# Performance work log

Hardware: AMD Instinct MI355X
Metric: run time of the kernel (lower is better)

## Reference

```python
import jax, jax.numpy as jnp
import numpy as np

D_X, D_H, N_I = 1024, 64, 16  # model dim, per-head dim (d_q=d_k=d_v), heads
BSZ, SEQ = 2, 2048


def _linear(x, W, b):
    return x @ W.T + b


def setup_inputs() -> dict:
    key = jax.random.key(0)
    ks = jax.random.split(key, 16)
    s_in = 1.0 / np.sqrt(D_X)
    s_hd = 1.0 / np.sqrt(N_I * D_H)
    return {
        "query": jax.random.normal(ks[0], (BSZ, SEQ, D_X), jnp.float32),
        "key": jax.random.normal(ks[1], (BSZ, SEQ, D_X), jnp.float32),
        "value": jax.random.normal(ks[2], (BSZ, SEQ, D_X), jnp.float32),
        "Wq": jax.random.normal(ks[3], (N_I * D_H, D_X), jnp.float32) * s_in,
        "bq": jnp.zeros((N_I * D_H,), jnp.float32),
        "Wk": jax.random.normal(ks[4], (N_I * D_H, D_X), jnp.float32) * s_in,
        "bk": jnp.zeros((N_I * D_H,), jnp.float32),
        "Wv": jax.random.normal(ks[5], (N_I * D_H, D_X), jnp.float32) * s_in,
        "bv": jnp.zeros((N_I * D_H,), jnp.float32),
        "Wxv": jax.random.normal(ks[6], (N_I * D_H, D_X), jnp.float32) * s_in,
        "bxv": jnp.zeros((N_I * D_H,), jnp.float32),
        "Wxo": jax.random.normal(ks[7], (D_X, N_I * D_H), jnp.float32) * s_hd,
        "bxo": jnp.zeros((D_X,), jnp.float32),
        "Wmo": jax.random.normal(ks[8], (D_X, N_I * D_H), jnp.float32) * s_hd,
        "bmo": jnp.zeros((D_X,), jnp.float32),
    }


def reference(query, key, value, Wq, bq, Wk, bk, Wv, bv, Wxv, bxv, Wxo, bxo, Wmo, bmo):
    bsz, seq, _ = query.shape

    def heads(x):  # (b, s, n_I*d) -> (b, h, s, d)
        return x.reshape(bsz, seq, N_I, D_H).transpose(0, 2, 1, 3)

    Q = heads(_linear(query, Wq, bq))
    K = heads(_linear(key, Wk, bk))
    V = heads(_linear(value, Wv, bv))

    dot = jnp.einsum('bhid,bhjd->bhij', Q, K) / jnp.sqrt(jnp.float32(D_H))
    attention = jax.nn.softmax(dot, axis=-1)  # dropout p=0 (eval)

    # use_xv=True: replace K with xV = W_xv(key) for the k_bar aggregation
    xV = heads(_linear(key, Wxv, bxv))

    k_bar = jnp.einsum('bhjd,bhij->bhid', xV, attention)
    v_bar = jnp.einsum('bhjd,bhij->bhid', V, attention)

    def merge(x):  # (b, h, s, d) -> (b, s, h*d)
        return x.transpose(0, 2, 1, 3).reshape(bsz, seq, N_I * D_H)

    x = _linear(merge(k_bar), Wxo, bxo)
    m = _linear(merge(v_bar), Wmo, bmo)
    return (x, m)
```

## Files before the change

kernel.cpp:

```cpp
#include <hip/hip_runtime.h>
#include <math.h>

typedef __bf16 bf16;
typedef __bf16 bf16x2 __attribute__((ext_vector_type(2)));
typedef __bf16 bf16x4 __attribute__((ext_vector_type(4)));
typedef __bf16 bf16x8 __attribute__((ext_vector_type(8)));
typedef float f32x4 __attribute__((ext_vector_type(4)));

#define SEQ 2048
#define DH 64
#define DX 1024
#define NH 16
#define LP 72

static __device__ __forceinline__ f32x4 mfma16(bf16x8 a, bf16x8 b, f32x4 c) {
    return __builtin_amdgcn_mfma_f32_16x16x32_bf16(a, b, c, 0, 0, 0);
}
static __device__ __forceinline__ bf16x8 cvt8(const float* __restrict__ p) {
    f32x4 a = *(const f32x4*)p;
    f32x4 b = *(const f32x4*)(p + 4);
    bf16x8 r;
    #pragma unroll
    for (int j = 0; j < 4; ++j) { r[j] = (bf16)a[j]; r[4 + j] = (bf16)b[j]; }
    return r;
}

#define GL16(gp, lp) __builtin_amdgcn_global_load_lds( \
    (const __attribute__((address_space(1))) void*)(gp), \
    (__attribute__((address_space(3))) void*)(lp), 16, 0, 0)


__global__ __launch_bounds__(256) void cvt_all(
    const float* __restrict__ q, const float* __restrict__ k,
    const float* __restrict__ v,
    const float* __restrict__ w0, const float* __restrict__ w1,
    const float* __restrict__ w2, const float* __restrict__ w3,
    const float* __restrict__ w4, const float* __restrict__ w5,
    bf16* __restrict__ out)
{
    const size_t i = (size_t)blockIdx.x * 2048 + threadIdx.x * 8;
    const int seg = (int)(i >> 20);
    const float* s;
    size_t off;
    if (seg < 4)       { s = q; off = i; }
    else if (seg < 8)  { s = k; off = i - (4ull << 20); }
    else if (seg < 12) { s = v; off = i - (8ull << 20); }
    else {
        const float* ww[6] = {w0, w1, w2, w3, w4, w5};
        s = ww[seg - 12]; off = i - ((size_t)seg << 20);
    }
    *(bf16x8*)(out + i) = cvt8(s + off);
}

struct G4 {
    const bf16* X[4]; const bf16* W[4]; const float* B[4];
    bf16* Yb[4]; float* Yf[4]; int xmode[4]; int ymode[4];
};

template<int BM>
__global__ __launch_bounds__(512) void gemm256(G4 a)
{
    constexpr int MREP = BM / 32;
    constexpr int NT   = DX / 64;
    constexpr int AEL  = BM * 64;
    constexpr int BEL  = 256 * 64;
    constexpr int SN   = BM / 64 + 4;
    __shared__ __align__(16) bf16 smem[2 * AEL + 2 * BEL];

    const int z = blockIdx.z;
    const bf16* __restrict__ X = a.X[z];
    const bf16* __restrict__ W = a.W[z];
    const int xmode = a.xmode[z], ymode = a.ymode[z];

    const int tid  = threadIdx.x;
    const int wid  = tid >> 6;
    const int lane = tid & 63;
    const int l16  = lane & 15;
    const int quad = lane >> 4;
    const int wm   = wid >> 2;
    const int wn   = wid & 3;

    const int nx = gridDim.x;
    const int nt = nx * gridDim.y;
    int t = blockIdx.x + nx * blockIdx.y;
    t = (t & 7) * (nt >> 3) + (t >> 3);
    const int n0 = (t % nx) * 256;
    const int m0 = (t / nx) * BM;

    const int srow8 = lane >> 3;
    const int sch   = (lane & 7) ^ srow8;

    f32x4 acc[MREP][4];
    #pragma unroll
    for (int i = 0; i < MREP; ++i)
        #pragma unroll
        for (int j = 0; j < 4; ++j) acc[i][j] = (f32x4){0.f,0.f,0.f,0.f};

    auto stage = [&](int buf, int kb) {
        bf16* Ab = smem + buf * AEL;
        bf16* Bb = smem + 2 * AEL + buf * BEL;
        #pragma unroll
        for (int g = 0; g < BM / 64; ++g) {
            const int row = g * 64 + wid * 8 + srow8;
            const bf16* src;
            if (xmode == 0) {
                src = X + (size_t)(m0 + row) * DX + kb * 64 + sch * 8;
            } else {
                const int m = m0 + row;
                const int b = m >> 11, s = m & 2047;
                src = X + ((size_t)(b * NH + kb) * SEQ + s) * DH + sch * 8;
            }
            GL16(src, Ab + (g * 64 + wid * 8) * 64);
        }
        #pragma unroll
        for (int g = 0; g < 4; ++g) {
            const int row = g * 64 + wid * 8 + srow8;
            const bf16* src = W + (size_t)(n0 + row) * DX + kb * 64 + sch * 8;
            GL16(src, Bb + (g * 64 + wid * 8) * 64);
        }
    };

    stage(0, 0);

    int cur = 0;
    for (int kb = 0; kb < NT; ++kb) {
        if (kb + 1 < NT) {
            stage(cur ^ 1, kb + 1);
            if constexpr (SN == 8) {
                __asm__ volatile("s_waitcnt vmcnt(8)" ::: "memory");
            } else {
                __asm__ volatile("s_waitcnt vmcnt(6)" ::: "memory");
            }
        } else {
            __asm__ volatile("s_waitcnt vmcnt(0)" ::: "memory");
        }
        __builtin_amdgcn_s_barrier();
        __builtin_amdgcn_sched_barrier(0);

        const bf16* Ab = smem + cur * AEL;
        const bf16* Bb = smem + 2 * AEL + cur * BEL;
        #pragma unroll
        for (int ks = 0; ks < 2; ++ks) {
            bf16x8 af[MREP], bfr[4];
            const int cc = (ks * 4 + quad) ^ (l16 & 7);
            #pragma unroll
            for (int mf = 0; mf < MREP; ++mf)
                af[mf] = *(const bf16x8*)&Ab[(wm * (BM/2) + mf * 16 + l16) * 64 + cc * 8];
            #pragma unroll
            for (int nf = 0; nf < 4; ++nf)
                bfr[nf] = *(const bf16x8*)&Bb[(wn * 64 + nf * 16 + l16) * 64 + cc * 8];
            #pragma unroll
            for (int mf = 0; mf < MREP; ++mf)
                #pragma unroll
                for (int nf = 0; nf < 4; ++nf)
                    acc[mf][nf] = mfma16(af[mf], bfr[nf], acc[mf][nf]);
        }
        __builtin_amdgcn_sched_barrier(0);
        __builtin_amdgcn_s_barrier();
        cur ^= 1;
    }

    if (ymode == 0) {
        constexpr int EPS = 264;
        constexpr int PR  = 128;
        constexpr int NP  = BM / PR;
        bf16* Ep = smem;
        #pragma unroll
        for (int p = 0; p < NP; ++p) {
            __builtin_amdgcn_s_barrier();
            if (NP == 1 || wm == p) {
                #pragma unroll
                for (int nf = 0; nf < 4; ++nf) {
                    const int col = wn * 64 + nf * 16 + l16;
                    const float bvv = a.B[z][n0 + col];
                    #pragma unroll
                    for (int mf = 0; mf < MREP; ++mf) {
                        const int rb = wm * (BM/2) + mf * 16 + quad * 4 - p * PR;
                        #pragma unroll
                        for (int r = 0; r < 4; ++r)
                            Ep[(rb + r) * EPS + col] = (bf16)(acc[mf][nf][r] + bvv);
                    }
                }
            }
            __asm__ volatile("s_waitcnt lgkmcnt(0)" ::: "memory");
            __builtin_amdgcn_s_barrier();
            #pragma unroll
            for (int j = 0; j < 8; ++j) {
                const int g    = j * 512 + tid;
                const int lrow = g >> 5;
                const int cg   = g & 31;
                bf16x8 vv = *(const bf16x8*)&Ep[lrow * EPS + cg * 8];
                const int row = m0 + p * PR + lrow;
                const int b = row >> 11, s = row & 2047;
                const int col = n0 + cg * 8;
                const int h = col >> 6, d = col & 63;
                *(bf16x8*)&a.Yb[z][((size_t)(b * NH + h) * SEQ + s) * DH + d] = vv;
            }
        }
    } else {
        #pragma unroll
        for (int nf = 0; nf < 4; ++nf) {
            const int col = n0 + wn * 64 + nf * 16 + l16;
            const float bvv = a.B[z][col];
            #pragma unroll
            for (int mf = 0; mf < MREP; ++mf) {
                #pragma unroll
                for (int r = 0; r < 4; ++r) {
                    const int row = m0 + wm * (BM/2) + mf * 16 + quad * 4 + r;
                    a.Yf[z][(size_t)row * DX + col] = acc[mf][nf][r] + bvv;
                }
            }
        }
    }
}

__global__ __launch_bounds__(512) void attn_pair(
    bf16* __restrict__ Q, const bf16* __restrict__ K,
    const bf16* __restrict__ V, const bf16* __restrict__ xV,
    bf16* __restrict__ VB)
{
    __shared__ __align__(16) bf16 Ks[2][64 * 64];
    __shared__ __align__(16) bf16 Vt [64 * LP];
    __shared__ __align__(16) bf16 xVt[64 * LP];
    __shared__ __align__(16) bf16 Pl[4][32 * LP];

    const int tid  = threadIdx.x;
    const int wid  = tid >> 6;
    const int lane = tid & 63;
    const int l16  = lane & 15;
    const int quad = lane >> 4;
    const int pair = wid >> 1;
    const int half = wid & 1;
    const size_t hb = ((size_t)blockIdx.z * NH + blockIdx.y) * SEQ * DH;
    const int qp = blockIdx.x * 128 + pair * 32;
    const int q0 = qp + half * 16;

    bf16x8 qf[2];
    #pragma unroll
    for (int ks = 0; ks < 2; ++ks)
        qf[ks] = *(const bf16x8*)(Q + hb + (size_t)(q0 + l16) * DH + ks*32 + quad*8);

    bf16x8 one8;
    #pragma unroll
    for (int j = 0; j < 8; ++j) one8[j] = (bf16)1.0f;

    f32x4 ov[2][4];
    f32x4 rsa[2];
    #pragma unroll
    for (int mf = 0; mf < 2; ++mf) {
        rsa[mf] = (f32x4){0.f,0.f,0.f,0.f};
        #pragma unroll
        for (int c = 0; c < 4; ++c) ov[mf][c] = (f32x4){0.f,0.f,0.f,0.f};
    }

    const int krow = lane >> 3;
    const int kch  = (lane & 7) ^ krow;
    const bf16* __restrict__ vsrc = (tid & 256) ? xV : V;
    bf16* __restrict__ vdst = (tid & 256) ? xVt : Vt;
    const int t8  = tid & 255;
    const int vkp = (t8 & 31) * 2;
    const int vd0 = (t8 >> 5) * 8;
    const float SCL = 0.125f * 1.4426950408889634f;

    bf16x8 pv0, pv1;
    {
        const bf16* kg = K + hb + (size_t)(wid*8 + krow) * DH + kch*8;
        GL16(kg, &Ks[0][(wid*8) * 64]);
        const size_t g0 = hb + (size_t)vkp * DH + vd0;
        pv0 = *(const bf16x8*)(vsrc + g0);
        pv1 = *(const bf16x8*)(vsrc + g0 + DH);
    }

    int c = 0;
    for (int kt = 0; kt < SEQ; kt += 64) {
        #pragma unroll
        for (int j = 0; j < 8; ++j)
            *(bf16x2*)&vdst[(vd0 + j) * LP + vkp] = (bf16x2){pv0[j], pv1[j]};
        if (kt + 64 < SEQ) {
            const bf16* kg = K + hb + (size_t)(kt + 64 + wid*8 + krow) * DH + kch*8;
            GL16(kg, &Ks[c ^ 1][(wid*8) * 64]);
            const size_t g0 = hb + (size_t)(kt + 64 + vkp) * DH + vd0;
            pv0 = *(const bf16x8*)(vsrc + g0);
            pv1 = *(const bf16x8*)(vsrc + g0 + DH);
        }
        __asm__ volatile("s_waitcnt lgkmcnt(0)" ::: "memory");
        __asm__ volatile("s_waitcnt vmcnt(3)" ::: "memory");
        __builtin_amdgcn_s_barrier();
        __builtin_amdgcn_sched_barrier(0);

        f32x4 sf[4];
        #pragma unroll
        for (int mf = 0; mf < 4; ++mf) sf[mf] = (f32x4){0.f,0.f,0.f,0.f};
        __builtin_amdgcn_s_setprio(1);
        #pragma unroll
        for (int ks = 0; ks < 2; ++ks)
            #pragma unroll
            for (int mf = 0; mf < 4; ++mf) {
                bf16x8 kf = *(const bf16x8*)&Ks[c][(mf*16 + l16) * 64 +
                                                   (((ks*4 + quad) ^ (l16 & 7)) * 8)];
                sf[mf] = mfma16(kf, qf[ks], sf[mf]);
            }
        __builtin_amdgcn_s_setprio(0);

        #pragma unroll
        for (int mf = 0; mf < 4; ++mf) {
            float p0 = __builtin_amdgcn_exp2f(sf[mf][0] * SCL);
            float p1 = __builtin_amdgcn_exp2f(sf[mf][1] * SCL);
            float p2 = __builtin_amdgcn_exp2f(sf[mf][2] * SCL);
            float p3 = __builtin_amdgcn_exp2f(sf[mf][3] * SCL);
            *(bf16x4*)&Pl[pair][(half*16 + l16) * LP + mf*16 + quad*4] =
                (bf16x4){(bf16)p0, (bf16)p1, (bf16)p2, (bf16)p3};
        }
        __asm__ volatile("s_waitcnt lgkmcnt(0)" ::: "memory");
        __builtin_amdgcn_s_barrier();
        __builtin_amdgcn_sched_barrier(0);

        __builtin_amdgcn_s_setprio(1);
        #pragma unroll
        for (int ks = 0; ks < 2; ++ks) {
            bf16x8 pa[2];
            #pragma unroll
            for (int mf = 0; mf < 2; ++mf)
                pa[mf] = *(const bf16x8*)&Pl[pair][(mf*16 + l16) * LP + ks*32 + quad*8];
            #pragma unroll
            for (int mf = 0; mf < 2; ++mf)
                rsa[mf] = mfma16(pa[mf], one8, rsa[mf]);
            const bf16* __restrict__ tile = half ? xVt : Vt;
            #pragma unroll
            for (int cc = 0; cc < 4; ++cc) {
                bf16x8 bv = *(const bf16x8*)&tile[(cc*16 + l16) * LP + ks*32 + quad*8];
                #pragma unroll
                for (int mf = 0; mf < 2; ++mf)
                    ov[mf][cc] = mfma16(pa[mf], bv, ov[mf][cc]);
            }
        }
        __builtin_amdgcn_s_setprio(0);

        __builtin_amdgcn_sched_barrier(0);
        __builtin_amdgcn_s_barrier();
        c ^= 1;
    }

    bf16* __restrict__ outp = half ? Q : VB;
    #pragma unroll
    for (int mf = 0; mf < 2; ++mf)
        #pragma unroll
        for (int r = 0; r < 4; ++r) {
            const int qrow = mf * 16 + quad * 4 + r;
            const float inv = 1.0f / rsa[mf][r];
            const size_t base = hb + (size_t)(qp + qrow) * DH;
            #pragma unroll
            for (int cc = 0; cc < 4; ++cc)
                outp[base + cc*16 + l16] = (bf16)(ov[mf][cc][r] * inv);
        }
}


__global__ __launch_bounds__(256) void proj_gemm(
    const void* __restrict__ Xv, const float* __restrict__ W,
    const float* __restrict__ bias, void* __restrict__ Yv,
    int in_kind, int out_mode)
{
    __shared__ __align__(16) bf16 As[64 * LP];
    __shared__ __align__(16) bf16 Bs[128 * LP];
    const int tid  = threadIdx.x;
    const int wave = tid >> 6;
    const int lane = tid & 63;
    const int l16  = lane & 15;
    const int quad = lane >> 4;
    const int m0 = blockIdx.y * 64;
    const int n0 = blockIdx.x * 128;
    const int m_w = (wave >> 1) * 32;
    const int n_w = (wave & 1) * 64;
    const int ar = tid >> 2, ac = (tid & 3) * 16;
    const int br = tid >> 1, bc = (tid & 1) * 32;

    f32x4 acc[2][4];
    #pragma unroll
    for (int i = 0; i < 2; ++i)
        #pragma unroll
        for (int j = 0; j < 4; ++j) acc[i][j] = (f32x4){0.f,0.f,0.f,0.f};

    for (int kb = 0; kb < DX / 64; ++kb) {
        __syncthreads();
        if (in_kind == 0) {
            const float* xp = (const float*)Xv + (size_t)(m0 + ar) * DX + kb * 64 + ac;
            *(bf16x8*)&As[ar * LP + ac]     = cvt8(xp);
            *(bf16x8*)&As[ar * LP + ac + 8] = cvt8(xp + 8);
        } else {
            const bf16* xp = (const bf16*)Xv + ((size_t)kb * SEQ + (m0 + ar)) * DH + ac;
            *(bf16x8*)&As[ar * LP + ac]     = *(const bf16x8*)xp;
            *(bf16x8*)&As[ar * LP + ac + 8] = *(const bf16x8*)(xp + 8);
        }
        {
            const float* wp = W + (size_t)(n0 + br) * DX + kb * 64 + bc;
            #pragma unroll
            for (int g = 0; g < 4; ++g)
                *(bf16x8*)&Bs[br * LP + bc + g * 8] = cvt8(wp + g * 8);
        }
        __syncthreads();
        #pragma unroll
        for (int ks = 0; ks < 2; ++ks) {
            bf16x8 a0 = *(const bf16x8*)&As[(m_w + l16)      * LP + ks * 32 + quad * 8];
            bf16x8 a1 = *(const bf16x8*)&As[(m_w + 16 + l16) * LP + ks * 32 + quad * 8];
            #pragma unroll
            for (int nf = 0; nf < 4; ++nf) {
                bf16x8 b = *(const bf16x8*)&Bs[(n_w + nf * 16 + l16) * LP + ks * 32 + quad * 8];
                acc[0][nf] = mfma16(a0, b, acc[0][nf]);
                acc[1][nf] = mfma16(a1, b, acc[1][nf]);
            }
        }
    }
    #pragma unroll
    for (int mf = 0; mf < 2; ++mf)
        #pragma unroll
        for (int nf = 0; nf < 4; ++nf) {
            const int col = n0 + n_w + nf * 16 + l16;
            const float bvv = bias[col];
            #pragma unroll
            for (int r = 0; r < 4; ++r) {
                const int row = m0 + m_w + mf * 16 + quad * 4 + r;
                float v = acc[mf][nf][r] + bvv;
                if (out_mode == 0) {
                    int h = col >> 6, d = col & 63;
                    ((bf16*)Yv)[((size_t)h * SEQ + row) * DH + d] = (bf16)v;
                } else {
                    ((float*)Yv)[(size_t)row * DX + col] = v;
                }
            }
        }
}

__global__ __launch_bounds__(256) void attn_dual(
    bf16* __restrict__ Q, const bf16* __restrict__ K,
    const bf16* __restrict__ V, const bf16* __restrict__ xV,
    bf16* __restrict__ vb)
{
    __shared__ __align__(16) bf16 Ks [64 * LP];
    __shared__ __align__(16) bf16 Vt [64 * LP];
    __shared__ __align__(16) bf16 xVt[64 * LP];
    __shared__ __align__(16) bf16 Pl[4][32 * LP];
    const int tid  = threadIdx.x;
    const int h    = blockIdx.y;
    const int qt   = blockIdx.x;
    const int wave = tid >> 6;
    const int lane = tid & 63;
    const int l16  = lane & 15;
    const int quad = lane >> 4;
    const size_t hb = (size_t)h * SEQ * DH;
    const int q0 = qt * 128 + wave * 32;

    bf16x8 qf[2][2];
    #pragma unroll
    for (int mf = 0; mf < 2; ++mf)
        #pragma unroll
        for (int ks = 0; ks < 2; ++ks)
            qf[mf][ks] = *(const bf16x8*)(Q + hb + (size_t)(q0 + mf*16 + l16) * DH + ks*32 + quad*8);

    float mr[2][4], lr[2][4];
    f32x4 ov[2][4], oxv[2][4];
    #pragma unroll
    for (int mf = 0; mf < 2; ++mf)
        #pragma unroll
        for (int r = 0; r < 4; ++r) { mr[mf][r] = -1e30f; lr[mf][r] = 0.f; }
    #pragma unroll
    for (int mf = 0; mf < 2; ++mf)
        #pragma unroll
        for (int c = 0; c < 4; ++c) {
            ov[mf][c]  = (f32x4){0.f,0.f,0.f,0.f};
            oxv[mf][c] = (f32x4){0.f,0.f,0.f,0.f};
        }
    const int sr = tid >> 2, sc = (tid & 3) * 16;
    const int vkp = (tid & 31) * 2;
    const int vd0 = (tid >> 5) * 8;
    const float SCL = 0.125f * 1.4426950408889634f;

    for (int kt = 0; kt < SEQ; kt += 64) {
        __syncthreads();
        {
            const bf16* kpt = K + hb + (size_t)(kt + sr) * DH + sc;
            *(bf16x8*)&Ks[sr * LP + sc]     = *(const bf16x8*)kpt;
            *(bf16x8*)&Ks[sr * LP + sc + 8] = *(const bf16x8*)(kpt + 8);
            const size_t g0 = hb + (size_t)(kt + vkp) * DH + vd0;
            bf16x8 v0 = *(const bf16x8*)(V + g0);
            bf16x8 v1 = *(const bf16x8*)(V + g0 + DH);
            bf16x8 x0 = *(const bf16x8*)(xV + g0);
            bf16x8 x1 = *(const bf16x8*)(xV + g0 + DH);
            #pragma unroll
            for (int j = 0; j < 8; ++j) {
                *(bf16x2*)&Vt [(vd0 + j) * LP + vkp] = (bf16x2){v0[j], v1[j]};
                *(bf16x2*)&xVt[(vd0 + j) * LP + vkp] = (bf16x2){x0[j], x1[j]};
            }
        }
        __syncthreads();
        f32x4 sf[2][4];
        #pragma unroll
        for (int mf = 0; mf < 2; ++mf)
            #pragma unroll
            for (int nf = 0; nf < 4; ++nf) sf[mf][nf] = (f32x4){0.f,0.f,0.f,0.f};
        #pragma unroll
        for (int ks = 0; ks < 2; ++ks)
            #pragma unroll
            for (int nf = 0; nf < 4; ++nf) {
                bf16x8 bk = *(const bf16x8*)&Ks[(nf * 16 + l16) * LP + ks * 32 + quad * 8];
                sf[0][nf] = mfma16(qf[0][ks], bk, sf[0][nf]);
                sf[1][nf] = mfma16(qf[1][ks], bk, sf[1][nf]);
            }
        float mx[2][4], rs[2][4], alpha[2][4];
        #pragma unroll
        for (int mf = 0; mf < 2; ++mf)
            #pragma unroll
            for (int r = 0; r < 4; ++r) {
                float aa = fmaxf(sf[mf][0][r], sf[mf][1][r]);
                float bb = fmaxf(sf[mf][2][r], sf[mf][3][r]);
                mx[mf][r] = fmaxf(aa, bb) * SCL;
            }
        #pragma unroll
        for (int off = 1; off < 16; off <<= 1)
            #pragma unroll
            for (int mf = 0; mf < 2; ++mf)
                #pragma unroll
                for (int r = 0; r < 4; ++r)
                    mx[mf][r] = fmaxf(mx[mf][r], __shfl_xor(mx[mf][r], off, 64));
        #pragma unroll
        for (int mf = 0; mf < 2; ++mf)
            #pragma unroll
            for (int r = 0; r < 4; ++r) {
                float mnew = fmaxf(mr[mf][r], mx[mf][r]);
                alpha[mf][r] = exp2f(mr[mf][r] - mnew);
                mr[mf][r] = mnew;
            }
        bf16* pw = &Pl[wave][0];
        #pragma unroll
        for (int mf = 0; mf < 2; ++mf)
            #pragma unroll
            for (int r = 0; r < 4; ++r) rs[mf][r] = 0.f;
        #pragma unroll
        for (int mf = 0; mf < 2; ++mf)
            #pragma unroll
            for (int nf = 0; nf < 4; ++nf)
                #pragma unroll
                for (int r = 0; r < 4; ++r) {
                    float p = exp2f(sf[mf][nf][r] * SCL - mr[mf][r]);
                    rs[mf][r] += p;
                    pw[(mf * 16 + quad * 4 + r) * LP + nf * 16 + l16] = (bf16)p;
                }
        #pragma unroll
        for (int off = 1; off < 16; off <<= 1)
            #pragma unroll
            for (int mf = 0; mf < 2; ++mf)
                #pragma unroll
                for (int r = 0; r < 4; ++r)
                    rs[mf][r] += __shfl_xor(rs[mf][r], off, 64);
        #pragma unroll
        for (int mf = 0; mf < 2; ++mf)
            #pragma unroll
            for (int r = 0; r < 4; ++r)
                lr[mf][r] = lr[mf][r] * alpha[mf][r] + rs[mf][r];
        #pragma unroll
        for (int mf = 0; mf < 2; ++mf)
            #pragma unroll
            for (int c = 0; c < 4; ++c)
                #pragma unroll
                for (int r = 0; r < 4; ++r) {
                    ov[mf][c][r]  *= alpha[mf][r];
                    oxv[mf][c][r] *= alpha[mf][r];
                }
        __asm__ volatile("s_waitcnt lgkmcnt(0)" ::: "memory");
        #pragma unroll
        for (int ks = 0; ks < 2; ++ks) {
            bf16x8 pa0 = *(const bf16x8*)&Pl[wave][(l16)      * LP + ks * 32 + quad * 8];
            bf16x8 pa1 = *(const bf16x8*)&Pl[wave][(16 + l16) * LP + ks * 32 + quad * 8];
            #pragma unroll
            for (int c = 0; c < 4; ++c) {
                bf16x8 bv = *(const bf16x8*)&Vt [(c * 16 + l16) * LP + ks * 32 + quad * 8];
                ov[0][c]  = mfma16(pa0, bv, ov[0][c]);
                ov[1][c]  = mfma16(pa1, bv, ov[1][c]);
                bf16x8 bx = *(const bf16x8*)&xVt[(c * 16 + l16) * LP + ks * 32 + quad * 8];
                oxv[0][c] = mfma16(pa0, bx, oxv[0][c]);
                oxv[1][c] = mfma16(pa1, bx, oxv[1][c]);
            }
        }
    }
    #pragma unroll
    for (int mf = 0; mf < 2; ++mf)
        #pragma unroll
        for (int r = 0; r < 4; ++r) {
            const int s = q0 + mf * 16 + quad * 4 + r;
            const float inv = 1.0f / lr[mf][r];
            #pragma unroll
            for (int c = 0; c < 4; ++c) {
                const int d = c * 16 + l16;
                Q [hb + (size_t)s * DH + d] = (bf16)(oxv[mf][c][r] * inv);
                vb[hb + (size_t)s * DH + d] = (bf16)(ov[mf][c][r]  * inv);
            }
        }
}


extern "C" void kernel_launch(void* const* d_in, const int* in_sizes, int n_in,
                              void* d_out, int out_size, void* d_ws, size_t ws_size,
                              hipStream_t stream) {
    const float* query = (const float*)d_in[0];
    const float* key   = (const float*)d_in[1];
    const float* value = (const float*)d_in[2];
    const float* Wq  = (const float*)d_in[3];  const float* bq  = (const float*)d_in[4];
    const float* Wk  = (const float*)d_in[5];  const float* bk  = (const float*)d_in[6];
    const float* Wv  = (const float*)d_in[7];  const float* bv  = (const float*)d_in[8];
    const float* Wxv = (const float*)d_in[9];  const float* bxv = (const float*)d_in[10];
    const float* Wxo = (const float*)d_in[11]; const float* bxo = (const float*)d_in[12];
    const float* Wmo = (const float*)d_in[13]; const float* bmo = (const float*)d_in[14];

    float* out = (float*)d_out;
    const size_t SB = (size_t)SEQ * DX;
    const size_t M1 = 1ull << 20;

    dim3 blk(256);

    if (ws_size >= (76ull << 20)) {
        bf16* ws = (bf16*)d_ws;
        bf16* qb  = ws;
        bf16* kb  = ws + 4 * M1;
        bf16* vb  = ws + 8 * M1;
        bf16* Wqb = ws + 12 * M1;
        bf16* Wkb = Wqb + M1;
        bf16* Wvb = Wkb + M1;
        bf16* Wxvb= Wvb + M1;
        bf16* Wxob= Wxvb + M1;
        bf16* Wmob= Wxob + M1;
        bf16* Qs  = ws + 18 * M1;
        bf16* Kss = ws + 22 * M1;
        bf16* Vs  = ws + 26 * M1;
        bf16* xVs = ws + 30 * M1;
        bf16* VBs = ws + 34 * M1;

        cvt_all<<<9216, blk, 0, stream>>>(query, key, value,
                                          Wq, Wk, Wv, Wxv, Wxo, Wmo, ws + 0);

        G4 g1;
        g1.X[0]=qb;  g1.W[0]=Wqb;  g1.B[0]=bq;  g1.Yb[0]=Qs;  g1.Yf[0]=nullptr; g1.xmode[0]=0; g1.ymode[0]=0;
        g1.X[1]=kb;  g1.W[1]=Wkb;  g1.B[1]=bk;  g1.Yb[1]=Kss; g1.Yf[1]=nullptr; g1.xmode[1]=0; g1.ymode[1]=0;
        g1.X[2]=vb;  g1.W[2]=Wvb;  g1.B[2]=bv;  g1.Yb[2]=Vs;  g1.Yf[2]=nullptr; g1.xmode[2]=0; g1.ymode[2]=0;
        g1.X[3]=kb;  g1.W[3]=Wxvb; g1.B[3]=bxv; g1.Yb[3]=xVs; g1.Yf[3]=nullptr; g1.xmode[3]=0; g1.ymode[3]=0;
        gemm256<256><<<dim3(4, 16, 4), dim3(512), 0, stream>>>(g1);

        attn_pair<<<dim3(16, NH, 2), dim3(512), 0, stream>>>(Qs, Kss, Vs, xVs, VBs);

        G4 g2;
        g2.X[0]=Qs;  g2.W[0]=Wxob; g2.B[0]=bxo; g2.Yb[0]=nullptr; g2.Yf[0]=out;          g2.xmode[0]=1; g2.ymode[0]=1;
        g2.X[1]=VBs; g2.W[1]=Wmob; g2.B[1]=bmo; g2.Yb[1]=nullptr; g2.Yf[1]=out + 2*SB;   g2.xmode[1]=1; g2.ymode[1]=1;
        g2.X[2]=Qs;  g2.W[2]=Wxob; g2.B[2]=bxo; g2.Yb[2]=nullptr; g2.Yf[2]=out;          g2.xmode[2]=1; g2.ymode[2]=1;
        g2.X[3]=Qs;  g2.W[3]=Wxob; g2.B[3]=bxo; g2.Yb[3]=nullptr; g2.Yf[3]=out;          g2.xmode[3]=1; g2.ymode[3]=1;
        gemm256<128><<<dim3(4, 32, 2), dim3(512), 0, stream>>>(g2);
    } else {
        bf16* Qs  = (bf16*)d_ws;
        bf16* Ksb = Qs  + SB;
        bf16* Vs  = Ksb + SB;
        bf16* xVs = Vs  + SB;
        bf16* vbs = xVs + SB;
        dim3 pg(8, 32);
        dim3 ag(16, NH);
        for (int b = 0; b < 2; ++b) {
            const float* q_b = query + (size_t)b * SB;
            const float* k_b = key   + (size_t)b * SB;
            const float* v_b = value + (size_t)b * SB;
            float* x_b = out + (size_t)b * SB;
            float* m_b = out + 2 * SB + (size_t)b * SB;
            proj_gemm<<<pg, blk, 0, stream>>>(q_b, Wq,  bq,  Qs,  0, 0);
            proj_gemm<<<pg, blk, 0, stream>>>(k_b, Wk,  bk,  Ksb, 0, 0);
            proj_gemm<<<pg, blk, 0, stream>>>(v_b, Wv,  bv,  Vs,  0, 0);
            proj_gemm<<<pg, blk, 0, stream>>>(k_b, Wxv, bxv, xVs, 0, 0);
            attn_dual<<<ag, blk, 0, stream>>>(Qs, Ksb, Vs, xVs, vbs);
            proj_gemm<<<pg, blk, 0, stream>>>(Qs,  Wxo, bxo, x_b, 1, 1);
            proj_gemm<<<pg, blk, 0, stream>>>(vbs, Wmo, bmo, m_b, 1, 1);
        }
    }
}
```

Before: 265.5 us.

## Software-pipeline attention loop so PV of previous tile overlaps QK of current

Restructures the attention main loop into a skewed pipeline. Each iteration computes QK scores and exponentials for tile i while running the P·V MFMAs for tile i-1 out of LDS, then writes P and the transposed V for tile i after one barrier, with a drain step after the loop. This cuts the number of barriers per iteration from three to two and lets the exp/convert work overlap with MFMA work. In exchange, registers must hold the packed P values and the next V prefetch, and the vmcnt wait is now vmcnt(0).

After: 257.3 us. 3.1% less time.

```diff
diff --git a/kernel.cpp b/kernel.cpp
--- a/kernel.cpp
+++ b/kernel.cpp
@@ -250,7 +250,7 @@
     for (int mf = 0; mf < 2; ++mf) {
         rsa[mf] = (f32x4){0.f,0.f,0.f,0.f};
         #pragma unroll
-        for (int c = 0; c < 4; ++c) ov[mf][c] = (f32x4){0.f,0.f,0.f,0.f};
+        for (int c2 = 0; c2 < 4; ++c2) ov[mf][c2] = (f32x4){0.f,0.f,0.f,0.f};
     }
 
     const int krow = lane >> 3;
@@ -262,29 +262,19 @@
     const int vd0 = (t8 >> 5) * 8;
     const float SCL = 0.125f * 1.4426950408889634f;
 
-    bf16x8 pv0, pv1;
+    bf16x8 cv0, cv1;
     {
         const bf16* kg = K + hb + (size_t)(wid*8 + krow) * DH + kch*8;
         GL16(kg, &Ks[0][(wid*8) * 64]);
         const size_t g0 = hb + (size_t)vkp * DH + vd0;
-        pv0 = *(const bf16x8*)(vsrc + g0);
-        pv1 = *(const bf16x8*)(vsrc + g0 + DH);
+        cv0 = *(const bf16x8*)(vsrc + g0);
+        cv1 = *(const bf16x8*)(vsrc + g0 + DH);
     }
 
     int c = 0;
-    for (int kt = 0; kt < SEQ; kt += 64) {
-        #pragma unroll
-        for (int j = 0; j < 8; ++j)
-            *(bf16x2*)&vdst[(vd0 + j) * LP + vkp] = (bf16x2){pv0[j], pv1[j]};
-        if (kt + 64 < SEQ) {
-            const bf16* kg = K + hb + (size_t)(kt + 64 + wid*8 + krow) * DH + kch*8;
-            GL16(kg, &Ks[c ^ 1][(wid*8) * 64]);
-            const size_t g0 = hb + (size_t)(kt + 64 + vkp) * DH + vd0;
-            pv0 = *(const bf16x8*)(vsrc + g0);
-            pv1 = *(const bf16x8*)(vsrc + g0 + DH);
-        }
-        __asm__ volatile("s_waitcnt lgkmcnt(0)" ::: "memory");
-        __asm__ volatile("s_waitcnt vmcnt(3)" ::: "memory");
+    for (int i = 0; i < SEQ / 64; ++i) {
+        const int kt = i * 64;
+        __asm__ volatile("s_waitcnt vmcnt(0)" ::: "memory");
         __builtin_amdgcn_s_barrier();
         __builtin_amdgcn_sched_barrier(0);
 
@@ -302,19 +292,67 @@
             }
         __builtin_amdgcn_s_setprio(0);
 
+        bf16x8 nv0, nv1;
+        const bool more = (i + 1 < SEQ / 64);
+        if (more) {
+            const bf16* kg = K + hb + (size_t)(kt + 64 + wid*8 + krow) * DH + kch*8;
+            GL16(kg, &Ks[c ^ 1][(wid*8) * 64]);
+            const size_t g0 = hb + (size_t)(kt + 64 + vkp) * DH + vd0;
+            nv0 = *(const bf16x8*)(vsrc + g0);
+            nv1 = *(const bf16x8*)(vsrc + g0 + DH);
+        }
+
+        bf16x4 pk[4];
         #pragma unroll
         for (int mf = 0; mf < 4; ++mf) {
             float p0 = __builtin_amdgcn_exp2f(sf[mf][0] * SCL);
             float p1 = __builtin_amdgcn_exp2f(sf[mf][1] * SCL);
             float p2 = __builtin_amdgcn_exp2f(sf[mf][2] * SCL);
             float p3 = __builtin_amdgcn_exp2f(sf[mf][3] * SCL);
-            *(bf16x4*)&Pl[pair][(half*16 + l16) * LP + mf*16 + quad*4] =
-                (bf16x4){(bf16)p0, (bf16)p1, (bf16)p2, (bf16)p3};
-        }
-        __asm__ volatile("s_waitcnt lgkmcnt(0)" ::: "memory");
+            pk[mf] = (bf16x4){(bf16)p0, (bf16)p1, (bf16)p2, (bf16)p3};
+        }
+
+        if (i > 0) {
+            __builtin_amdgcn_s_setprio(1);
+            #pragma unroll
+            for (int ks = 0; ks < 2; ++ks) {
+                bf16x8 pa[2];
+                #pragma unroll
+                for (int mf = 0; mf < 2; ++mf)
+                    pa[mf] = *(const bf16x8*)&Pl[pair][(mf*16 + l16) * LP + ks*32 + quad*8];
+                #pragma unroll
+                for (int mf = 0; mf < 2; ++mf)
+                    rsa[mf] = mfma16(pa[mf], one8, rsa[mf]);
+                const bf16* __restrict__ tile = half ? xVt : Vt;
+                #pragma unroll
+                for (int cc = 0; cc < 4; ++cc) {
+                    bf16x8 bv = *(const bf16x8*)&tile[(cc*16 + l16) * LP + ks*32 + quad*8];
+                    #pragma unroll
+                    for (int mf = 0; mf < 2; ++mf)
+                        ov[mf][cc] = mfma16(pa[mf], bv, ov[mf][cc]);
+                }
+            }
+            __builtin_amdgcn_s_setprio(0);
+        }
+
+        __builtin_amdgcn_sched_barrier(0);
         __builtin_amdgcn_s_barrier();
         __builtin_amdgcn_sched_barrier(0);
 
+        #pragma unroll
+        for (int mf = 0; mf < 4; ++mf)
+            *(bf16x4*)&Pl[pair][(half*16 + l16) * LP + mf*16 + quad*4] = pk[mf];
+        #pragma unroll
+        for (int j = 0; j < 8; ++j)
+            *(bf16x2*)&vdst[(vd0 + j) * LP + vkp] = (bf16x2){cv0[j], cv1[j]};
+        __asm__ volatile("s_waitcnt lgkmcnt(0)" ::: "memory");
+        if (more) { cv0 = nv0; cv1 = nv1; }
+        c ^= 1;
+    }
+
+    __builtin_amdgcn_s_barrier();
+    __builtin_amdgcn_sched_barrier(0);
+    {
         __builtin_amdgcn_s_setprio(1);
         #pragma unroll
         for (int ks = 0; ks < 2; ++ks) {
@@ -335,10 +373,6 @@
             }
         }
         __builtin_amdgcn_s_setprio(0);
-
-        __builtin_amdgcn_sched_barrier(0);
-        __builtin_amdgcn_s_barrier();
-        c ^= 1;
     }
 
     bf16* __restrict__ outp = half ? Q : VB;
```
